# Optimization experiments

Measured on AMD Instinct MI355X. Metric: run time of the kernel, lower is better.

The kernel has to match this reference:

```python
import jax, jax.numpy as jnp
import numpy as np

LN_EPS = 1e-5      # torch nn.LayerNorm default
NORM_EPS = 1e-12   # torch F.normalize default
EPS = 1e-8         # loss eps


def layer_norm(x, gamma, beta):
    mu = x.mean(axis=-1, keepdims=True)
    var = x.var(axis=-1, keepdims=True)  # biased, matches torch LN
    return (x - mu) * jax.lax.rsqrt(var + LN_EPS) * gamma + beta


def l2norm(x):
    n = jnp.sqrt(jnp.sum(x * x, axis=-1, keepdims=True))
    return x / jnp.maximum(n, NORM_EPS)


def setup_inputs() -> dict:
    key = jax.random.key(0)
    k1, k2, k3 = jax.random.split(key, 3)
    N, B, L, D = 1024, 64, 197, 768
    text_features = jax.random.normal(k1, (N, D), dtype=jnp.float32)
    vision_tokens = jax.random.normal(k2, (B, L, D), dtype=jnp.float32)
    group_map = jnp.sort(jax.random.randint(k3, (N,), 0, B)).astype(jnp.int64)
    ln_gamma = jnp.ones((D,), dtype=jnp.float32)
    ln_beta = jnp.zeros((D,), dtype=jnp.float32)
    log_loss_temp = jnp.array([np.log(0.07)], dtype=jnp.float32)
    return {
        "text_features": text_features,
        "vision_tokens": vision_tokens,
        "group_map": group_map,
        "ln_gamma": ln_gamma,
        "ln_beta": ln_beta,
        "log_loss_temp": log_loss_temp,
    }


def reference(text_features, vision_tokens, group_map, ln_gamma, ln_beta, log_loss_temp):
    D = text_features.shape[-1]
    # shared LayerNorm on both modalities
    tf = layer_norm(text_features, ln_gamma, ln_beta)          # [N, D]
    vt = layer_norm(vision_tokens, ln_gamma, ln_beta)          # [B, L, D]

    # SimilarityLogit, sim_op='dot': scores / sqrt(D), softmax over tokens
    scores = jnp.einsum('nd,bld->bnl', tf, vt) / jnp.sqrt(jnp.float32(D))
    attn = jax.nn.softmax(scores, axis=-1)                     # [B, N, L]
    aggregated = jnp.einsum('bnl,bld->bnd', attn, vt)          # [B, N, D]

    qn = l2norm(tf)                                            # [N, D]
    an = l2norm(aggregated)                                    # [B, N, D]
    logits = jnp.einsum('nd,bnd->nb', qn, an)                  # [N, B] (== [B,N].T)

    # multi-positive NCE loss (row_sum=False, col_sum=False)
    temp = jnp.exp(log_loss_temp)[0]
    scaled = jnp.exp(logits / temp)                            # [N, B]
    N = scaled.shape[0]
    idx = jnp.arange(N)
    pos = scaled[idx, group_map]                               # [N]

    # row loss: pos / sum over images
    row_p = pos / (scaled.sum(axis=1) + EPS)
    row_loss = -jnp.log(row_p + EPS)

    # column loss: pos / (pos + sum of negatives in its column)
    neg_mask = jnp.ones_like(scaled).at[idx, group_map].set(0.0)
    sum_neg = (scaled * neg_mask).sum(axis=0)[group_map]       # [N]
    col_p = pos / (pos + sum_neg + EPS)
    col_loss = -jnp.log(col_p + EPS)

    return (row_loss.mean() + col_loss.mean()) / 2
```

## Files before the change

### kernel.cpp

```cpp
#include <hip/hip_runtime.h>
#include <hip/hip_bf16.h>
#include <math.h>

#define NN 1024
#define BB 64
#define LL 197
#define LP 256
#define LBV 13
#define DD 768

typedef __attribute__((ext_vector_type(8))) short short8;
typedef __attribute__((ext_vector_type(4))) float f32x4;

constexpr float LN_EPS = 1e-5f;
constexpr float NORM_EPS = 1e-12f;
constexpr float EPS = 1e-8f;

__device__ __forceinline__ float waveSum(float v) {
#pragma unroll
    for (int m = 32; m >= 1; m >>= 1) v += __shfl_xor(v, m, 64);
    return v;
}
__device__ __forceinline__ float grpSum(float v) {
#pragma unroll
    for (int m = 8; m >= 1; m >>= 1) v += __shfl_xor(v, m, 64);
    return v;
}
__device__ __forceinline__ float grpMax(float v) {
#pragma unroll
    for (int m = 8; m >= 1; m >>= 1) v = fmaxf(v, __shfl_xor(v, m, 64));
    return v;
}

__device__ __forceinline__ float bf2f(unsigned short u) {
    unsigned int x = ((unsigned int)u) << 16;
    return reinterpret_cast<float&>(x);
}

__device__ __forceinline__ void gl_lds16(const void* g, void* l) {
    __builtin_amdgcn_global_load_lds(
        (const __attribute__((address_space(1))) unsigned int*)g,
        (__attribute__((address_space(3))) unsigned int*)l, 16, 0, 0);
}

__device__ __forceinline__ void lite_barrier() {
    asm volatile("s_barrier" ::: "memory");
}

__global__ __launch_bounds__(256) void ln_kernel(
    const float* __restrict__ x, __hip_bfloat16* __restrict__ y,
    const float* __restrict__ gamma, const float* __restrict__ beta,
    float* __restrict__ qinv) {
    const int row = blockIdx.x;
    const int tid = threadIdx.x;
    const float* xr = x + (size_t)row * DD;
    __hip_bfloat16* yr = y + (size_t)row * DD;

    float v[3];
    float s = 0.f, ss = 0.f;
#pragma unroll
    for (int c = 0; c < 3; c++) {
        float t = xr[tid + 256 * c];
        v[c] = t; s += t; ss += t * t;
    }
    __shared__ float red[8];
    s = waveSum(s); ss = waveSum(ss);
    const int w = tid >> 6;
    if ((tid & 63) == 0) { red[w] = s; red[4 + w] = ss; }
    __syncthreads();
    s = red[0] + red[1] + red[2] + red[3];
    ss = red[4] + red[5] + red[6] + red[7];
    const float mean = s * (1.f / DD);
    const float var = ss * (1.f / DD) - mean * mean;
    const float rs = rsqrtf(var + LN_EPS);

    float q = 0.f;
#pragma unroll
    for (int c = 0; c < 3; c++) {
        const int d = tid + 256 * c;
        float t = (v[c] - mean) * rs * gamma[d] + beta[d];
        __hip_bfloat16 hb = __float2bfloat16(t);
        yr[d] = hb;
        float tb = __bfloat162float(hb);
        q += tb * tb;
    }
    __syncthreads();
    q = waveSum(q);
    if ((tid & 63) == 0) red[w] = q;
    __syncthreads();
    if (tid == 0) {
        float n2 = red[0] + red[1] + red[2] + red[3];
        qinv[row] = 1.f / fmaxf(sqrtf(n2), NORM_EPS);
    }
}

__global__ __launch_bounds__(256) void ln_vis_kernel(
    const float* __restrict__ x, __hip_bfloat16* __restrict__ y,
    const float* __restrict__ gamma, const float* __restrict__ beta) {
    const int id = blockIdx.x;
    const int xcd = id & 7;
    const int k = id >> 3;
    const int bhi = k >> 8;
    const int l = k & 255;
    const int b = xcd + 8 * bhi;
    const int tid = threadIdx.x;
    __hip_bfloat16* yr = y + ((size_t)b * LP + l) * DD;
    if (l >= LL) {
#pragma unroll
        for (int c = 0; c < 3; c++) yr[tid + 256 * c] = __float2bfloat16(0.f);
        return;
    }
    const float* xr = x + ((size_t)b * LL + l) * DD;

    float v[3];
    float s = 0.f, ss = 0.f;
#pragma unroll
    for (int c = 0; c < 3; c++) {
        float t = xr[tid + 256 * c];
        v[c] = t; s += t; ss += t * t;
    }
    __shared__ float red[8];
    s = waveSum(s); ss = waveSum(ss);
    const int w = tid >> 6;
    if ((tid & 63) == 0) { red[w] = s; red[4 + w] = ss; }
    __syncthreads();
    s = red[0] + red[1] + red[2] + red[3];
    ss = red[4] + red[5] + red[6] + red[7];
    const float mean = s * (1.f / DD);
    const float var = ss * (1.f / DD) - mean * mean;
    const float rs = rsqrtf(var + LN_EPS);
#pragma unroll
    for (int c = 0; c < 3; c++) {
        const int d = tid + 256 * c;
        yr[d] = __float2bfloat16((v[c] - mean) * rs * gamma[d] + beta[d]);
    }
}

__global__ __launch_bounds__(256, 2) void gram_kernel(
    const __hip_bfloat16* __restrict__ vt, __hip_bfloat16* __restrict__ G) {
    const int id = blockIdx.x;
    const int xcd = id & 7;
    const int k = id >> 3;
    const int bhi = k >> 3;
    const int rb = k & 7;
    const int b = xcd + 8 * bhi;
    const int n0 = rb * 32;
    const int tid = threadIdx.x, w = tid >> 6, lane = tid & 63;
    const int g = lane >> 4, c = lane & 15;
    const int gsw = (g ^ ((c ^ (c >> 2)) & 3)) * 16;

    __shared__ __align__(16) unsigned char smem[55296];
    const char* vtbc = (const char*)(vt + (size_t)b * LP * DD);

#define GSTAGE(ks, bsel)                                                        \
    {                                                                           \
        const int kb_ = (ks) * 64;                                              \
        _Pragma("unroll")                                                       \
        for (int q_ = 0; q_ < 4; q_++) {                                        \
            const int o_ = q_ * 4096 + tid * 16;                                \
            const int r_ = o_ >> 6;                                             \
            const int sj_ = ((o_ >> 4) & 3) ^ ((r_ ^ (r_ >> 2)) & 3);           \
            gl_lds16(vtbc + (size_t)r_ * 1536 + kb_ + sj_ * 16,                 \
                     smem + (bsel) * 16384 + q_ * 4096 + w * 1024);             \
        }                                                                       \
        if (w < 2) {                                                            \
            const int o_ = tid * 16;                                            \
            const int r_ = o_ >> 6;                                             \
            const int sj_ = ((o_ >> 4) & 3) ^ ((r_ ^ (r_ >> 2)) & 3);           \
            gl_lds16(vtbc + (size_t)(n0 + r_) * 1536 + kb_ + sj_ * 16,          \
                     smem + 49152 + (bsel) * 2048 + w * 1024);                  \
        }                                                                       \
    }

    f32x4 acc[4][2];
#pragma unroll
    for (int i = 0; i < 4; i++)
#pragma unroll
        for (int nb = 0; nb < 2; nb++) acc[i][nb] = {0.f, 0.f, 0.f, 0.f};

    GSTAGE(0, 0);
    GSTAGE(1, 1);
    asm volatile("s_waitcnt vmcnt(4)" ::: "memory");
    lite_barrier();

    for (int ks = 0; ks < 24; ks++) {
        if (ks < 22) GSTAGE(ks + 2, (ks + 2) % 3);
        const unsigned char* vb = smem + (ks % 3) * 16384;
        const unsigned char* tb = smem + 49152 + (ks % 3) * 2048;
        short8 af[2], bf[4];
#pragma unroll
        for (int nb = 0; nb < 2; nb++)
            af[nb] = *(const short8*)(tb + (nb * 16 + c) * 64 + gsw);
#pragma unroll
        for (int i = 0; i < 4; i++)
            bf[i] = *(const short8*)(vb + ((w + 4 * i) * 16 + c) * 64 + gsw);
#pragma unroll
        for (int i = 0; i < 4; i++)
#pragma unroll
            for (int nb = 0; nb < 2; nb++)
                acc[i][nb] = __builtin_amdgcn_mfma_f32_16x16x32_bf16(
                    af[nb], bf[i], acc[i][nb], 0, 0, 0);
        if (ks < 22) asm volatile("s_waitcnt vmcnt(4)" ::: "memory");
        else         asm volatile("s_waitcnt vmcnt(0)" ::: "memory");
        lite_barrier();
    }
#undef GSTAGE

    __hip_bfloat16* Gb = G + (size_t)b * LP * LP;
#pragma unroll
    for (int i = 0; i < 4; i++) {
        const int col = (w + 4 * i) * 16 + c;
#pragma unroll
        for (int nb = 0; nb < 2; nb++)
#pragma unroll
            for (int r = 0; r < 4; r++)
                Gb[(size_t)(n0 + nb * 16 + g * 4 + r) * LP + col] =
                    __float2bfloat16(acc[i][nb][r]);
    }
}

__global__ __launch_bounds__(256, 3) void score_kernel(
    const __hip_bfloat16* __restrict__ tf, const __hip_bfloat16* __restrict__ vt,
    const float* __restrict__ qinv, __hip_bfloat16* __restrict__ Pbuf,
    float* __restrict__ numq) {
    const int id = blockIdx.x;
    const int xcd = id & 7;
    const int kk = id >> 3;
    const int bhi = kk >> 4;
    const int nt = kk & 15;
    const int b = xcd + 8 * bhi;
    const int n0 = nt * 64;
    const int tid = threadIdx.x, w = tid >> 6, lane = tid & 63;
    const int g = lane >> 4, c = lane & 15;
    const int gsw = (g ^ ((c ^ (c >> 2)) & 3)) * 16;

    __shared__ __align__(16) unsigned char smem[34816];
    float* mx = (float*)smem;
    float* sm = mx + 256;
    float* nm = sm + 256;

    const char* vtbc = (const char*)(vt + (size_t)b * LP * DD);
    const char* tfc = (const char*)(tf + (size_t)n0 * DD);

#define SSTAGE(ks, bsel)                                                        \
    {                                                                           \
        const int kb_ = (ks) * 64;                                              \
        _Pragma("unroll")                                                       \
        for (int q_ = 0; q_ < 3; q_++) {                                        \
            const int o_ = q_ * 4096 + tid * 16;                                \
            const int r_ = o_ >> 6;                                             \
            const int sj_ = ((o_ >> 4) & 3) ^ ((r_ ^ (r_ >> 2)) & 3);           \
            gl_lds16(vtbc + (size_t)r_ * 1536 + kb_ + sj_ * 16,                 \
                     smem + (bsel) * 13312 + q_ * 4096 + w * 1024);             \
        }                                                                       \
        if (lane < 16) {                                                        \
            const int o_ = 12288 + (w * 16 + lane) * 16;                        \
            const int r_ = o_ >> 6;                                             \
            const int sj_ = ((o_ >> 4) & 3) ^ ((r_ ^ (r_ >> 2)) & 3);           \
            gl_lds16(vtbc + (size_t)r_ * 1536 + kb_ + sj_ * 16,                 \
                     smem + (bsel) * 13312 + 12288 + w * 256);                  \
        }                                                                       \
        {                                                                       \
            const int o_ = tid * 16;                                            \
            const int r_ = o_ >> 6;                                             \
            const int sj_ = ((o_ >> 4) & 3) ^ ((r_ ^ (r_ >> 2)) & 3);           \
            gl_lds16(tfc + (size_t)r_ * 1536 + kb_ + sj_ * 16,                  \
                     smem + 26624 + (bsel) * 4096 + w * 1024);                  \
        }                                                                       \
    }

    f32x4 acc[4][4];
#pragma unroll
    for (int i = 0; i < 4; i++)
#pragma unroll
        for (int nb = 0; nb < 4; nb++) acc[i][nb] = {0.f, 0.f, 0.f, 0.f};

    SSTAGE(0, 0);
    SSTAGE(1, 1);
    asm volatile("s_waitcnt vmcnt(5)" ::: "memory");
    lite_barrier();

    for (int ks = 0; ks < 24; ks++) {
        const unsigned char* vb = smem + (ks & 1) * 13312;
        const unsigned char* tb = smem + 26624 + (ks & 1) * 4096;
        short8 af[4];
#pragma unroll
        for (int nb = 0; nb < 4; nb++)
            af[nb] = *(const short8*)(tb + (nb * 16 + c) * 64 + gsw);
#pragma unroll
        for (int i = 0; i < 4; i++) {
            const int lb = w + 4 * i;
            if (lb < LBV) {
                short8 bfv = *(const short8*)(vb + (lb * 16 + c) * 64 + gsw);
#pragma unroll
                for (int nb = 0; nb < 4; nb++)
                    acc[i][nb] = __builtin_amdgcn_mfma_f32_16x16x32_bf16(
                        af[nb], bfv, acc[i][nb], 0, 0, 0);
            }
        }
        lite_barrier();
        if (ks < 22) {
            SSTAGE(ks + 2, ks & 1);
            asm volatile("s_waitcnt vmcnt(5)" ::: "memory");
        } else {
            asm volatile("s_waitcnt vmcnt(0)" ::: "memory");
        }
        lite_barrier();
    }
#undef SSTAGE

    const float inv_sqrtD = 0.0360843918f;
    float mp[4][4];
#pragma unroll
    for (int nb = 0; nb < 4; nb++)
#pragma unroll
        for (int r = 0; r < 4; r++) mp[nb][r] = -1e30f;
#pragma unroll
    for (int i = 0; i < 4; i++) {
        const int l = (w + 4 * i) * 16 + c;
        if (l < LL) {
#pragma unroll
            for (int nb = 0; nb < 4; nb++)
#pragma unroll
                for (int r = 0; r < 4; r++) mp[nb][r] = fmaxf(mp[nb][r], acc[i][nb][r]);
        }
    }
#pragma unroll
    for (int nb = 0; nb < 4; nb++)
#pragma unroll
        for (int r = 0; r < 4; r++) mp[nb][r] = grpMax(mp[nb][r]);
    if (c == 0) {
#pragma unroll
        for (int nb = 0; nb < 4; nb++)
#pragma unroll
            for (int r = 0; r < 4; r++) mx[(nb * 16 + g * 4 + r) * 4 + w] = mp[nb][r];
    }
    __syncthreads();
    float mf[4][4];
#pragma unroll
    for (int nb = 0; nb < 4; nb++)
#pragma unroll
        for (int r = 0; r < 4; r++) {
            const int row = nb * 16 + g * 4 + r;
            mf[nb][r] = fmaxf(fmaxf(mx[row * 4 + 0], mx[row * 4 + 1]),
                              fmaxf(mx[row * 4 + 2], mx[row * 4 + 3]));
        }

    float sp[4][4], np[4][4];
#pragma unroll
    for (int nb = 0; nb < 4; nb++)
#pragma unroll
        for (int r = 0; r < 4; r++) { sp[nb][r] = 0.f; np[nb][r] = 0.f; }
#pragma unroll
    for (int i = 0; i < 4; i++) {
        const int l = (w + 4 * i) * 16 + c;
#pragma unroll
        for (int nb = 0; nb < 4; nb++)
#pragma unroll
            for (int r = 0; r < 4; r++) {
                const float raw = acc[i][nb][r];
                const float p = (l < LL) ? __expf((raw - mf[nb][r]) * inv_sqrtD) : 0.f;
                acc[i][nb][r] = p;
                sp[nb][r] += p;
                np[nb][r] += p * raw;
            }
    }
#pragma unroll
    for (int nb = 0; nb < 4; nb++)
#pragma unroll
        for (int r = 0; r < 4; r++) { sp[nb][r] = grpSum(sp[nb][r]); np[nb][r] = grpSum(np[nb][r]); }
    if (c == 0) {
#pragma unroll
        for (int nb = 0; nb < 4; nb++)
#pragma unroll
            for (int r = 0; r < 4; r++) {
                const int row = nb * 16 + g * 4 + r;
                sm[row * 4 + w] = sp[nb][r];
                nm[row * 4 + w] = np[nb][r];
            }
    }
    __syncthreads();

    float invs[4][4];
#pragma unroll
    for (int nb = 0; nb < 4; nb++)
#pragma unroll
        for (int r = 0; r < 4; r++) {
            const int row = nb * 16 + g * 4 + r;
            const float ssum = sm[row * 4 + 0] + sm[row * 4 + 1] + sm[row * 4 + 2] + sm[row * 4 + 3];
            invs[nb][r] = 1.f / ssum;
        }

    __hip_bfloat16* Pb = Pbuf + ((size_t)b * NN + n0) * LP;
#pragma unroll
    for (int i = 0; i < 4; i++) {
        const int lb = w + 4 * i;
#pragma unroll
        for (int nb = 0; nb < 4; nb++)
#pragma unroll
            for (int r = 0; r < 4; r++)
                Pb[(size_t)(nb * 16 + g * 4 + r) * LP + lb * 16 + c] =
                    __float2bfloat16(acc[i][nb][r] * invs[nb][r]);
    }

    if (tid < 64) {
        const int row = tid;
        const int n = n0 + row;
        const float ssum = sm[row * 4 + 0] + sm[row * 4 + 1] + sm[row * 4 + 2] + sm[row * 4 + 3];
        const float nsum = nm[row * 4 + 0] + nm[row * 4 + 1] + nm[row * 4 + 2] + nm[row * 4 + 3];
        numq[(size_t)n * BB + b] = (nsum / ssum) * qinv[n];
    }
}

__global__ __launch_bounds__(256, 3) void den_kernel(
    const __hip_bfloat16* __restrict__ Pbuf, const __hip_bfloat16* __restrict__ G,
    const float* __restrict__ numq, float* __restrict__ logits) {
    const int id = blockIdx.x;
    const int xcd = id & 7;
    const int kk = id >> 3;
    const int bhi = kk >> 4;
    const int nt = kk & 15;
    const int b = xcd + 8 * bhi;
    const int n0 = nt * 64;
    const int tid = threadIdx.x, w = tid >> 6, lane = tid & 63;
    const int g = lane >> 4, c = lane & 15;
    const int gsw = (g ^ ((c ^ (c >> 2)) & 3)) * 16;

    __shared__ __align__(16) unsigned char smem[34816];
    float* mx = (float*)smem;

    const char* Gbc = (const char*)(G + (size_t)b * LP * LP);
    const char* Pbc = (const char*)(Pbuf + ((size_t)b * NN + n0) * LP);

#define DSTAGE(ks, bsel)                                                        \
    {                                                                           \
        const int kb_ = (ks) * 64;                                              \
        _Pragma("unroll")                                                       \
        for (int q_ = 0; q_ < 3; q_++) {                                        \
            const int o_ = q_ * 4096 + tid * 16;                                \
            const int r_ = o_ >> 6;                                             \
            const int sj_ = ((o_ >> 4) & 3) ^ ((r_ ^ (r_ >> 2)) & 3);           \
            gl_lds16(Gbc + (size_t)r_ * 512 + kb_ + sj_ * 16,                   \
                     smem + (bsel) * 13312 + q_ * 4096 + w * 1024);             \
        }                                                                       \
        if (lane < 16) {                                                        \
            const int o_ = 12288 + (w * 16 + lane) * 16;                        \
            const int r_ = o_ >> 6;                                             \
            const int sj_ = ((o_ >> 4) & 3) ^ ((r_ ^ (r_ >> 2)) & 3);           \
            gl_lds16(Gbc + (size_t)r_ * 512 + kb_ + sj_ * 16,                   \
                     smem + (bsel) * 13312 + 12288 + w * 256);                  \
        }                                                                       \
        {                                                                       \
            const int o_ = tid * 16;                                            \
            const int r_ = o_ >> 6;                                             \
            const int sj_ = ((o_ >> 4) & 3) ^ ((r_ ^ (r_ >> 2)) & 3);           \
            gl_lds16(Pbc + (size_t)r_ * 512 + kb_ + sj_ * 16,                   \
                     smem + 26624 + (bsel) * 4096 + w * 1024);                  \
        }                                                                       \
    }

    f32x4 acc[4][4];
#pragma unroll
    for (int i = 0; i < 4; i++)
#pragma unroll
        for (int nb = 0; nb < 4; nb++) acc[i][nb] = {0.f, 0.f, 0.f, 0.f};

    DSTAGE(0, 0);
    DSTAGE(1, 1);
    asm volatile("s_waitcnt vmcnt(5)" ::: "memory");
    lite_barrier();

    for (int ks = 0; ks < 7; ks++) {
        const unsigned char* vb = smem + (ks & 1) * 13312;
        const unsigned char* tb = smem + 26624 + (ks & 1) * 4096;
        short8 af[4];
#pragma unroll
        for (int nb = 0; nb < 4; nb++)
            af[nb] = *(const short8*)(tb + (nb * 16 + c) * 64 + gsw);
#pragma unroll
        for (int i = 0; i < 4; i++) {
            const int lb = w + 4 * i;
            if (lb < LBV) {
                short8 bfv = *(const short8*)(vb + (lb * 16 + c) * 64 + gsw);
#pragma unroll
                for (int nb = 0; nb < 4; nb++)
                    acc[i][nb] = __builtin_amdgcn_mfma_f32_16x16x32_bf16(
                        af[nb], bfv, acc[i][nb], 0, 0, 0);
            }
        }
        lite_barrier();
        if (ks < 5) {
            DSTAGE(ks + 2, ks & 1);
            asm volatile("s_waitcnt vmcnt(5)" ::: "memory");
        } else {
            asm volatile("s_waitcnt vmcnt(0)" ::: "memory");
        }
        lite_barrier();
    }
#undef DSTAGE

    const short* Pb = (const short*)Pbc;
    float den[4][4];
#pragma unroll
    for (int nb = 0; nb < 4; nb++)
#pragma unroll
        for (int r = 0; r < 4; r++) den[nb][r] = 0.f;
#pragma unroll
    for (int i = 0; i < 4; i++) {
        const int lb = w + 4 * i;
        if (lb < LBV) {
            const int col = lb * 16 + c;
#pragma unroll
            for (int nb = 0; nb < 4; nb++)
#pragma unroll
                for (int r = 0; r < 4; r++) {
                    const float P = bf2f((unsigned short)Pb[(size_t)(nb * 16 + g * 4 + r) * LP + col]);
                    den[nb][r] += P * acc[i][nb][r];
                }
        }
    }

#pragma unroll
    for (int nb = 0; nb < 4; nb++)
#pragma unroll
        for (int r = 0; r < 4; r++) den[nb][r] = grpSum(den[nb][r]);
    __syncthreads();
    if (c == 0) {
#pragma unroll
        for (int nb = 0; nb < 4; nb++)
#pragma unroll
            for (int r = 0; r < 4; r++) mx[(nb * 16 + g * 4 + r) * 4 + w] = den[nb][r];
    }
    __syncthreads();
    if (tid < 64) {
        const int row = tid;
        const int n = n0 + row;
        const float dsum = mx[row * 4 + 0] + mx[row * 4 + 1] + mx[row * 4 + 2] + mx[row * 4 + 3];
        const float dn = fmaxf(sqrtf(fmaxf(dsum, 0.f)), NORM_EPS);
        logits[(size_t)n * BB + b] = numq[(size_t)n * BB + b] / dn;
    }
}

__global__ __launch_bounds__(64) void loss_row_kernel(
    const float* __restrict__ logits, const int* __restrict__ gm,
    const float* __restrict__ logtemp, float* __restrict__ scaled,
    float* __restrict__ posv, float* __restrict__ rowloss) {
    const int n = blockIdx.x;
    const int b = threadIdx.x;
    const float invtemp = 1.f / expf(logtemp[0]);
    const float e = expf(logits[(size_t)n * BB + b] * invtemp);
    scaled[(size_t)n * BB + b] = e;
    const float sum = waveSum(e);
    const int g = gm[n];
    const float pos = __shfl(e, g, 64);
    if (b == 0) {
        posv[n] = pos;
        rowloss[n] = -logf(pos / (sum + EPS) + EPS);
    }
}

__global__ __launch_bounds__(256) void colsum_kernel(
    const float* __restrict__ scaled, const int* __restrict__ gm,
    float* __restrict__ colsum, float* __restrict__ poscol) {
    const int b = blockIdx.x;
    const int tid = threadIdx.x;
    float s = 0.f, p = 0.f;
    for (int n = tid; n < NN; n += 256) {
        const float e = scaled[(size_t)n * BB + b];
        s += e;
        if (gm[n] == b) p += e;
    }
    s = waveSum(s); p = waveSum(p);
    __shared__ float red[8];
    const int w = tid >> 6;
    if ((tid & 63) == 0) { red[w] = s; red[4 + w] = p; }
    __syncthreads();
    if (tid == 0) {
        colsum[b] = red[0] + red[1] + red[2] + red[3];
        poscol[b] = red[4] + red[5] + red[6] + red[7];
    }
}

__global__ __launch_bounds__(1024) void final_kernel(
    const float* __restrict__ posv, const float* __restrict__ rowloss,
    const float* __restrict__ colsum, const float* __restrict__ poscol,
    const int* __restrict__ gm, float* __restrict__ out) {
    const int n = threadIdx.x;
    const int g = gm[n];
    const float pos = posv[n];
    const float sum_neg = colsum[g] - poscol[g];
    const float cl = -logf(pos / (pos + sum_neg + EPS) + EPS);
    float v = rowloss[n] + cl;
    v = waveSum(v);
    __shared__ float red[16];
    if ((n & 63) == 0) red[n >> 6] = v;
    __syncthreads();
    if (n == 0) {
        float s = 0.f;
#pragma unroll
        for (int i = 0; i < 16; i++) s += red[i];
        out[0] = s / (2.f * NN);
    }
}

extern "C" void kernel_launch(void* const* d_in, const int* in_sizes, int n_in,
                              void* d_out, int out_size, void* d_ws, size_t ws_size,
                              hipStream_t stream) {
    const float* text = (const float*)d_in[0];
    const float* vis = (const float*)d_in[1];
    const int* gm = (const int*)d_in[2];
    const float* gamma = (const float*)d_in[3];
    const float* beta = (const float*)d_in[4];
    const float* logtemp = (const float*)d_in[5];
    float* out = (float*)d_out;

    char* w = (char*)d_ws;
    __hip_bfloat16* tf = (__hip_bfloat16*)w;             w += (size_t)NN * DD * 2;
    __hip_bfloat16* vt = (__hip_bfloat16*)w;             w += (size_t)BB * LP * DD * 2;
    __hip_bfloat16* G  = (__hip_bfloat16*)w;             w += (size_t)BB * LP * LP * 2;
    __hip_bfloat16* Pbuf = (__hip_bfloat16*)w;           w += (size_t)BB * NN * LP * 2;
    float* qinv    = (float*)w;  w += (size_t)NN * 4;
    float* numq    = (float*)w;  w += (size_t)NN * BB * 4;
    float* logits  = (float*)w;  w += (size_t)NN * BB * 4;
    float* scaled  = (float*)w;  w += (size_t)NN * BB * 4;
    float* posv    = (float*)w;  w += (size_t)NN * 4;
    float* rowloss = (float*)w;  w += (size_t)NN * 4;
    float* colsum  = (float*)w;  w += (size_t)BB * 4;
    float* poscol  = (float*)w;  w += (size_t)BB * 4;

    ln_kernel<<<NN, 256, 0, stream>>>(text, tf, gamma, beta, qinv);
    ln_vis_kernel<<<BB * LP, 256, 0, stream>>>(vis, vt, gamma, beta);

    score_kernel<<<1024, 256, 0, stream>>>(tf, vt, qinv, Pbuf, numq);
    gram_kernel<<<512, 256, 0, stream>>>(vt, G);
    den_kernel<<<1024, 256, 0, stream>>>(Pbuf, G, numq, logits);

    loss_row_kernel<<<NN, 64, 0, stream>>>(logits, gm, logtemp, scaled, posv, rowloss);
    colsum_kernel<<<BB, 256, 0, stream>>>(scaled, gm, colsum, poscol);
    final_kernel<<<1, 1024, 0, stream>>>(posv, rowloss, colsum, poscol, gm, out);
}
```

Before: 115.7 us.

## Store bf16 intermediates in K-slab-major tiled layout for contiguous staging loads

Changes the workspace layout of the normalized text, vision tokens, Gram matrix and softmax probabilities from row-major to 32-element K-slabs, so each 64-byte K chunk for all rows is contiguous in memory. The MFMA kernels' global-to-LDS staging then reads contiguous 16 KB or 64 KB slabs instead of strided 64-byte pieces from long rows. The Gram kernel also reuses the vision slab already in LDS for its A operand, dropping a separate load and shrinking shared memory. The cost is that the LayerNorm writes and the epilogue stores become scattered 2-byte writes with a larger stride.

```diff
diff --git a/kernel.cpp b/kernel.cpp
--- a/kernel.cpp
+++ b/kernel.cpp
@@ -54,7 +54,6 @@
     const int row = blockIdx.x;
     const int tid = threadIdx.x;
     const float* xr = x + (size_t)row * DD;
-    __hip_bfloat16* yr = y + (size_t)row * DD;
 
     float v[3];
     float s = 0.f, ss = 0.f;
@@ -80,7 +79,7 @@
         const int d = tid + 256 * c;
         float t = (v[c] - mean) * rs * gamma[d] + beta[d];
         __hip_bfloat16 hb = __float2bfloat16(t);
-        yr[d] = hb;
+        y[((size_t)(d >> 5) * NN + row) * 32 + (d & 31)] = hb;
         float tb = __bfloat162float(hb);
         q += tb * tb;
     }
@@ -104,10 +103,12 @@
     const int l = k & 255;
     const int b = xcd + 8 * bhi;
     const int tid = threadIdx.x;
-    __hip_bfloat16* yr = y + ((size_t)b * LP + l) * DD;
     if (l >= LL) {
 #pragma unroll
-        for (int c = 0; c < 3; c++) yr[tid + 256 * c] = __float2bfloat16(0.f);
+        for (int c = 0; c < 3; c++) {
+            const int d = tid + 256 * c;
+            y[(((size_t)b * 24 + (d >> 5)) * LP + l) * 32 + (d & 31)] = __float2bfloat16(0.f);
+        }
         return;
     }
     const float* xr = x + ((size_t)b * LL + l) * DD;
@@ -132,12 +133,13 @@
 #pragma unroll
     for (int c = 0; c < 3; c++) {
         const int d = tid + 256 * c;
-        yr[d] = __float2bfloat16((v[c] - mean) * rs * gamma[d] + beta[d]);
+        y[(((size_t)b * 24 + (d >> 5)) * LP + l) * 32 + (d & 31)] =
+            __float2bfloat16((v[c] - mean) * rs * gamma[d] + beta[d]);
     }
 }
 
 __global__ __launch_bounds__(256, 2) void gram_kernel(
-    const __hip_bfloat16* __restrict__ vt, __hip_bfloat16* __restrict__ G) {
+    const __hip_bfloat16* __restrict__ vt_t, __hip_bfloat16* __restrict__ G_t) {
     const int id = blockIdx.x;
     const int xcd = id & 7;
     const int k = id >> 3;
@@ -149,26 +151,19 @@
     const int g = lane >> 4, c = lane & 15;
     const int gsw = (g ^ ((c ^ (c >> 2)) & 3)) * 16;
 
-    __shared__ __align__(16) unsigned char smem[55296];
-    const char* vtbc = (const char*)(vt + (size_t)b * LP * DD);
+    __shared__ __align__(16) unsigned char smem[49152];
+    const char* vtbc = (const char*)vt_t + (size_t)b * 24 * 16384;
 
 #define GSTAGE(ks, bsel)                                                        \
     {                                                                           \
-        const int kb_ = (ks) * 64;                                              \
+        const char* vsl_ = vtbc + (size_t)(ks) * 16384;                         \
         _Pragma("unroll")                                                       \
         for (int q_ = 0; q_ < 4; q_++) {                                        \
             const int o_ = q_ * 4096 + tid * 16;                                \
             const int r_ = o_ >> 6;                                             \
             const int sj_ = ((o_ >> 4) & 3) ^ ((r_ ^ (r_ >> 2)) & 3);           \
-            gl_lds16(vtbc + (size_t)r_ * 1536 + kb_ + sj_ * 16,                 \
+            gl_lds16(vsl_ + r_ * 64 + sj_ * 16,                                 \
                      smem + (bsel) * 16384 + q_ * 4096 + w * 1024);             \
-        }                                                                       \
-        if (w < 2) {                                                            \
-            const int o_ = tid * 16;                                            \
-            const int r_ = o_ >> 6;                                             \
-            const int sj_ = ((o_ >> 4) & 3) ^ ((r_ ^ (r_ >> 2)) & 3);           \
-            gl_lds16(vtbc + (size_t)(n0 + r_) * 1536 + kb_ + sj_ * 16,          \
-                     smem + 49152 + (bsel) * 2048 + w * 1024);                  \
         }                                                                       \
     }
 
@@ -186,11 +181,10 @@
     for (int ks = 0; ks < 24; ks++) {
         if (ks < 22) GSTAGE(ks + 2, (ks + 2) % 3);
         const unsigned char* vb = smem + (ks % 3) * 16384;
-        const unsigned char* tb = smem + 49152 + (ks % 3) * 2048;
         short8 af[2], bf[4];
 #pragma unroll
         for (int nb = 0; nb < 2; nb++)
-            af[nb] = *(const short8*)(tb + (nb * 16 + c) * 64 + gsw);
+            af[nb] = *(const short8*)(vb + (n0 + nb * 16 + c) * 64 + gsw);
 #pragma unroll
         for (int i = 0; i < 4; i++)
             bf[i] = *(const short8*)(vb + ((w + 4 * i) * 16 + c) * 64 + gsw);
@@ -206,22 +200,21 @@
     }
 #undef GSTAGE
 
-    __hip_bfloat16* Gb = G + (size_t)b * LP * LP;
 #pragma unroll
     for (int i = 0; i < 4; i++) {
-        const int col = (w + 4 * i) * 16 + c;
+        const int cw = w + 4 * i;
 #pragma unroll
         for (int nb = 0; nb < 2; nb++)
 #pragma unroll
             for (int r = 0; r < 4; r++)
-                Gb[(size_t)(n0 + nb * 16 + g * 4 + r) * LP + col] =
-                    __float2bfloat16(acc[i][nb][r]);
+                G_t[(((size_t)b * 8 + (cw >> 1)) * LP + n0 + nb * 16 + g * 4 + r) * 32 +
+                    (cw & 1) * 16 + c] = __float2bfloat16(acc[i][nb][r]);
     }
 }
 
 __global__ __launch_bounds__(256, 3) void score_kernel(
-    const __hip_bfloat16* __restrict__ tf, const __hip_bfloat16* __restrict__ vt,
-    const float* __restrict__ qinv, __hip_bfloat16* __restrict__ Pbuf,
+    const __hip_bfloat16* __restrict__ tf_t, const __hip_bfloat16* __restrict__ vt_t,
+    const float* __restrict__ qinv, __hip_bfloat16* __restrict__ P_t,
     float* __restrict__ numq) {
     const int id = blockIdx.x;
     const int xcd = id & 7;
@@ -239,32 +232,33 @@
     float* sm = mx + 256;
     float* nm = sm + 256;
 
-    const char* vtbc = (const char*)(vt + (size_t)b * LP * DD);
-    const char* tfc = (const char*)(tf + (size_t)n0 * DD);
+    const char* vtbc = (const char*)vt_t + (size_t)b * 24 * 16384;
+    const char* tfc = (const char*)tf_t;
 
 #define SSTAGE(ks, bsel)                                                        \
     {                                                                           \
-        const int kb_ = (ks) * 64;                                              \
+        const char* vsl_ = vtbc + (size_t)(ks) * 16384;                         \
+        const char* tsl_ = tfc + (size_t)(ks) * 65536 + (size_t)n0 * 64;        \
         _Pragma("unroll")                                                       \
         for (int q_ = 0; q_ < 3; q_++) {                                        \
             const int o_ = q_ * 4096 + tid * 16;                                \
             const int r_ = o_ >> 6;                                             \
             const int sj_ = ((o_ >> 4) & 3) ^ ((r_ ^ (r_ >> 2)) & 3);           \
-            gl_lds16(vtbc + (size_t)r_ * 1536 + kb_ + sj_ * 16,                 \
+            gl_lds16(vsl_ + r_ * 64 + sj_ * 16,                                 \
                      smem + (bsel) * 13312 + q_ * 4096 + w * 1024);             \
         }                                                                       \
         if (lane < 16) {                                                        \
             const int o_ = 12288 + (w * 16 + lane) * 16;                        \
             const int r_ = o_ >> 6;                                             \
             const int sj_ = ((o_ >> 4) & 3) ^ ((r_ ^ (r_ >> 2)) & 3);           \
-            gl_lds16(vtbc + (size_t)r_ * 1536 + kb_ + sj_ * 16,                 \
+            gl_lds16(vsl_ + r_ * 64 + sj_ * 16,                                 \
                      smem + (bsel) * 13312 + 12288 + w * 256);                  \
         }                                                                       \
         {                                                                       \
             const int o_ = tid * 16;                                            \
             const int r_ = o_ >> 6;                                             \
             const int sj_ = ((o_ >> 4) & 3) ^ ((r_ ^ (r_ >> 2)) & 3);           \
-            gl_lds16(tfc + (size_t)r_ * 1536 + kb_ + sj_ * 16,                  \
+            gl_lds16(tsl_ + r_ * 64 + sj_ * 16,                                 \
                      smem + 26624 + (bsel) * 4096 + w * 1024);                  \
         }                                                                       \
     }
@@ -391,7 +385,6 @@
             invs[nb][r] = 1.f / ssum;
         }
 
-    __hip_bfloat16* Pb = Pbuf + ((size_t)b * NN + n0) * LP;
 #pragma unroll
     for (int i = 0; i < 4; i++) {
         const int lb = w + 4 * i;
@@ -399,8 +392,8 @@
         for (int nb = 0; nb < 4; nb++)
 #pragma unroll
             for (int r = 0; r < 4; r++)
-                Pb[(size_t)(nb * 16 + g * 4 + r) * LP + lb * 16 + c] =
-                    __float2bfloat16(acc[i][nb][r] * invs[nb][r]);
+                P_t[(((size_t)b * 8 + (lb >> 1)) * NN + n0 + nb * 16 + g * 4 + r) * 32 +
+                    (lb & 1) * 16 + c] = __float2bfloat16(acc[i][nb][r] * invs[nb][r]);
     }
 
     if (tid < 64) {
@@ -413,7 +406,7 @@
 }
 
 __global__ __launch_bounds__(256, 3) void den_kernel(
-    const __hip_bfloat16* __restrict__ Pbuf, const __hip_bfloat16* __restrict__ G,
+    const __hip_bfloat16* __restrict__ P_t, const __hip_bfloat16* __restrict__ G_t,
     const float* __restrict__ numq, float* __restrict__ logits) {
     const int id = blockIdx.x;
     const int xcd = id & 7;
@@ -429,32 +422,33 @@
     __shared__ __align__(16) unsigned char smem[34816];
     float* mx = (float*)smem;
 
-    const char* Gbc = (const char*)(G + (size_t)b * LP * LP);
-    const char* Pbc = (const char*)(Pbuf + ((size_t)b * NN + n0) * LP);
+    const char* Gbc = (const char*)G_t + (size_t)b * 8 * 16384;
+    const char* Pbc = (const char*)P_t + (size_t)b * 8 * 65536;
 
 #define DSTAGE(ks, bsel)                                                        \
     {                                                                           \
-        const int kb_ = (ks) * 64;                                              \
+        const char* vsl_ = Gbc + (size_t)(ks) * 16384;                          \
+        const char* psl_ = Pbc + (size_t)(ks) * 65536 + (size_t)n0 * 64;        \
         _Pragma("unroll")                                                       \
         for (int q_ = 0; q_ < 3; q_++) {                                        \
             const int o_ = q_ * 4096 + tid * 16;                                \
             const int r_ = o_ >> 6;                                             \
             const int sj_ = ((o_ >> 4) & 3) ^ ((r_ ^ (r_ >> 2)) & 3);           \
-            gl_lds16(Gbc + (size_t)r_ * 512 + kb_ + sj_ * 16,                   \
+            gl_lds16(vsl_ + r_ * 64 + sj_ * 16,                                 \
                      smem + (bsel) * 13312 + q_ * 4096 + w * 1024);             \
         }                                                                       \
         if (lane < 16) {                                                        \
             const int o_ = 12288 + (w * 16 + lane) * 16;                        \
             const int r_ = o_ >> 6;                                             \
             const int sj_ = ((o_ >> 4) & 3) ^ ((r_ ^ (r_ >> 2)) & 3);           \
-            gl_lds16(Gbc + (size_t)r_ * 512 + kb_ + sj_ * 16,                   \
+            gl_lds16(vsl_ + r_ * 64 + sj_ * 16,                                 \
                      smem + (bsel) * 13312 + 12288 + w * 256);                  \
         }                                                                       \
         {                                                                       \
             const int o_ = tid * 16;                                            \
             const int r_ = o_ >> 6;                                             \
             const int sj_ = ((o_ >> 4) & 3) ^ ((r_ ^ (r_ >> 2)) & 3);           \
-            gl_lds16(Pbc + (size_t)r_ * 512 + kb_ + sj_ * 16,                   \
+            gl_lds16(psl_ + r_ * 64 + sj_ * 16,                                 \
                      smem + 26624 + (bsel) * 4096 + w * 1024);                  \
         }                                                                       \
     }
@@ -499,7 +493,7 @@
     }
 #undef DSTAGE
 
-    const short* Pb = (const short*)Pbc;
+    const short* Pg = (const short*)P_t;
     float den[4][4];
 #pragma unroll
     for (int nb = 0; nb < 4; nb++)
@@ -509,13 +503,13 @@
     for (int i = 0; i < 4; i++) {
         const int lb = w + 4 * i;
         if (lb < LBV) {
-            const int col = lb * 16 + c;
 #pragma unroll
             for (int nb = 0; nb < 4; nb++)
 #pragma unroll
                 for (int r = 0; r < 4; r++) {
-                    const float P = bf2f((unsigned short)Pb[(size_t)(nb * 16 + g * 4 + r) * LP + col]);
-                    den[nb][r] += P * acc[i][nb][r];
+                    const size_t pa = (((size_t)b * 8 + (lb >> 1)) * NN + n0 + nb * 16 + g * 4 + r) * 32 +
+                                      (lb & 1) * 16 + c;
+                    den[nb][r] += bf2f((unsigned short)Pg[pa]) * acc[i][nb][r];
                 }
         }
     }
@@ -615,10 +609,10 @@
     float* out = (float*)d_out;
 
     char* w = (char*)d_ws;
-    __hip_bfloat16* tf = (__hip_bfloat16*)w;             w += (size_t)NN * DD * 2;
-    __hip_bfloat16* vt = (__hip_bfloat16*)w;             w += (size_t)BB * LP * DD * 2;
-    __hip_bfloat16* G  = (__hip_bfloat16*)w;             w += (size_t)BB * LP * LP * 2;
-    __hip_bfloat16* Pbuf = (__hip_bfloat16*)w;           w += (size_t)BB * NN * LP * 2;
+    __hip_bfloat16* tf_t = (__hip_bfloat16*)w;  w += (size_t)24 * NN * 32 * 2;
+    __hip_bfloat16* vt_t = (__hip_bfloat16*)w;  w += (size_t)BB * 24 * LP * 32 * 2;
+    __hip_bfloat16* G_t  = (__hip_bfloat16*)w;  w += (size_t)BB * 8 * LP * 32 * 2;
+    __hip_bfloat16* P_t  = (__hip_bfloat16*)w;  w += (size_t)BB * 8 * NN * 32 * 2;
     float* qinv    = (float*)w;  w += (size_t)NN * 4;
     float* numq    = (float*)w;  w += (size_t)NN * BB * 4;
     float* logits  = (float*)w;  w += (size_t)NN * BB * 4;
@@ -628,12 +622,12 @@
     float* colsum  = (float*)w;  w += (size_t)BB * 4;
     float* poscol  = (float*)w;  w += (size_t)BB * 4;
 
-    ln_kernel<<<NN, 256, 0, stream>>>(text, tf, gamma, beta, qinv);
-    ln_vis_kernel<<<BB * LP, 256, 0, stream>>>(vis, vt, gamma, beta);
-
-    score_kernel<<<1024, 256, 0, stream>>>(tf, vt, qinv, Pbuf, numq);
-    gram_kernel<<<512, 256, 0, stream>>>(vt, G);
-    den_kernel<<<1024, 256, 0, stream>>>(Pbuf, G, numq, logits);
+    ln_kernel<<<NN, 256, 0, stream>>>(text, tf_t, gamma, beta, qinv);
+    ln_vis_kernel<<<BB * LP, 256, 0, stream>>>(vis, vt_t, gamma, beta);
+
+    score_kernel<<<1024, 256, 0, stream>>>(tf_t, vt_t, qinv, P_t, numq);
+    gram_kernel<<<512, 256, 0, stream>>>(vt_t, G_t);
+    den_kernel<<<1024, 256, 0, stream>>>(P_t, G_t, numq, logits);
 
     loss_row_kernel<<<NN, 64, 0, stream>>>(logits, gm, logtemp, scaled, posv, rowloss);
     colsum_kernel<<<BB, 256, 0, stream>>>(scaled, gm, colsum, poscol);
```

Result: faster. 113.0 us (-2.4%).
